# Performance work log

Measured on AMD Instinct MI355X. Metric: run time of the kernel, lower is better.

Reference implementation:

```python
import jax, jax.numpy as jnp
import numpy as np

NEGPOS_RATIO = 3


def setup_inputs() -> dict:
    key = jax.random.key(0)
    k1, k2, k3 = jax.random.split(key, 3)
    B, P, NUM_ATTR, NUM_CLASSES = 64, 32768, 14, 10
    p = jax.random.normal(k1, (B, P, NUM_ATTR), dtype=jnp.float32)
    loc_t = jax.random.normal(k2, (B, P, 4), dtype=jnp.float32)
    conf_t = jax.random.randint(k3, (B, P), 0, NUM_CLASSES, dtype=jnp.int32)
    return {"p": p, "loc_t": loc_t, "conf_t": conf_t}


def reference(p, loc_t, conf_t):
    # p: [B, P, 4 + num_classes] concatenated loc + conf predictions
    loc_p = p[:, :, :4]
    conf_p = p[:, :, 4:]
    B, P = conf_t.shape

    pos = conf_t > 0                       # [B, P] positive anchor mask
    num_pos = jnp.sum(pos)                 # global scalar, as in original

    # Smooth-L1 (beta=1) summed over positive anchors
    diff = loc_p - loc_t
    ad = jnp.abs(diff)
    sl1 = jnp.where(ad < 1.0, 0.5 * diff * diff, ad - 0.5)
    loss_loc = jnp.sum(sl1 * pos[..., None].astype(sl1.dtype))

    # Per-anchor CE-style confidence loss: logsumexp - logit[target]
    lse = jax.nn.logsumexp(conf_p, axis=-1)                      # [B, P]
    tgt_logit = jnp.take_along_axis(conf_p, conf_t[..., None].astype(jnp.int32), axis=-1)[..., 0]
    ce_all = lse - tgt_logit                                     # [B, P]

    # Hard negative mining: zero positives, rank descending per image
    loss_c = jnp.where(pos, 0.0, ce_all)
    order = jnp.argsort(-loss_c, axis=1)   # descending sort indices
    rank = jnp.argsort(order, axis=1)      # rank of each anchor
    num_neg = jnp.clip(NEGPOS_RATIO * num_pos, None, P - num_pos)
    neg = rank < num_neg                   # [B, P]

    sel = pos | neg
    loss_c_sum = jnp.sum(ce_all * sel.astype(ce_all.dtype))

    return (loss_loc + loss_c_sum) / num_pos.astype(p.dtype)
```

## Files before the change

### kernel.cpp

```cpp
#include <hip/hip_runtime.h>

#define NB 64
#define NP 32768
#define NA 14
#define NC 10
#define NANCH (NB * NP)
#define TILE 256
#define TPB 4
#define MAIN_BLOCKS (NANCH / (TILE * TPB))

#define ACC_LOSS  (2 * MAIN_BLOCKS)
#define ACC_NPOS  (2 * MAIN_BLOCKS + 1)
#define DONE_SLOT (2 * MAIN_BLOCKS + 2)

typedef const __attribute__((address_space(1))) void* gptr_t;
typedef __attribute__((address_space(3))) void* lptr_t;

__global__ __launch_bounds__(256) void ssd_main(
    const float* __restrict__ p,
    const float* __restrict__ loc_t,
    const int* __restrict__ conf_t,
    double* __restrict__ ws)
{
    __shared__ float sp[2][TILE * NA];

    const int tid  = threadIdx.x;
    const int lane = tid & 63, wid = tid >> 6;
    const size_t tile0 = (size_t)blockIdx.x * TPB;

    auto stage = [&](int b, size_t tidx) {
        const char* gsrc  = reinterpret_cast<const char*>(p + tidx * (TILE * NA));
        char*       sbase = reinterpret_cast<char*>(sp[b]);
#pragma unroll
        for (int k = 0; k < 3; ++k) {
            const int c0 = k * 256 + wid * 64;
            __builtin_amdgcn_global_load_lds(
                (gptr_t)(gsrc + (size_t)(c0 + lane) * 16),
                (lptr_t)(sbase + (size_t)c0 * 16), 16, 0, 0);
        }
        if (wid < 2) {
            const int c0 = 768 + wid * 64;
            __builtin_amdgcn_global_load_lds(
                (gptr_t)(gsrc + (size_t)(c0 + lane) * 16),
                (lptr_t)(sbase + (size_t)c0 * 16), 16, 0, 0);
        }
    };

    stage(0, tile0);

    float lossAcc = 0.f;
    int   cntAcc  = 0;

#pragma unroll
    for (int it = 0; it < TPB; ++it) {
        const size_t abase = (tile0 + it) * TILE;
        float4 lt = reinterpret_cast<const float4*>(loc_t)[abase + tid];
        int t = conf_t[abase + tid];

        __syncthreads();

        if (it + 1 < TPB) stage((it + 1) & 1, tile0 + it + 1);

        const float2* row =
            reinterpret_cast<const float2*>(&sp[it & 1][tid * NA]);
        float x[14];
#pragma unroll
        for (int j = 0; j < 7; ++j) {
            float2 w = row[j];
            x[2 * j]     = w.x;
            x[2 * j + 1] = w.y;
        }

        float m = x[4];
#pragma unroll
        for (int j = 5; j < 14; ++j) m = fmaxf(m, x[j]);
        float s = 0.f;
#pragma unroll
        for (int j = 4; j < 14; ++j) s += __expf(x[j] - m);
        float lse = m + __logf(s);

        float tgt = x[4];
#pragma unroll
        for (int j = 1; j < 10; ++j) tgt = (t == j) ? x[4 + j] : tgt;
        float ce = lse - tgt;

        if (t > 0) {
            float l = ce;
            const float* ltf = reinterpret_cast<const float*>(&lt);
#pragma unroll
            for (int j = 0; j < 4; ++j) {
                float d  = x[j] - ltf[j];
                float ad = fabsf(d);
                l += (ad < 1.f) ? (0.5f * d * d) : (ad - 0.5f);
            }
            lossAcc += l;
            ++cntAcc;
        }
    }

    double dl = (double)lossAcc;
    int cnt = cntAcc;
#pragma unroll
    for (int off = 32; off > 0; off >>= 1) {
        dl  += __shfl_down(dl, off, 64);
        cnt += __shfl_down(cnt, off, 64);
    }
    __shared__ double sL[4];
    __shared__ int    sC[4];
    if (lane == 0) { sL[wid] = dl; sC[wid] = cnt; }
    __syncthreads();
    if (tid == 0) {
        ws[blockIdx.x] = sL[0] + sL[1] + sL[2] + sL[3];
        ws[MAIN_BLOCKS + blockIdx.x] =
            (double)(sC[0] + sC[1] + sC[2] + sC[3]);
    }
}

__global__ __launch_bounds__(256) void ssd_reduce(double* __restrict__ ws,
                                                  float* __restrict__ out)
{
    const int tid = threadIdx.x;
    double l = 0.0, c = 0.0;
    for (int i = tid; i < MAIN_BLOCKS; i += 256) {
        l += ws[i];
        c += ws[MAIN_BLOCKS + i];
    }
#pragma unroll
    for (int off = 32; off > 0; off >>= 1) {
        l += __shfl_down(l, off, 64);
        c += __shfl_down(c, off, 64);
    }
    __shared__ double sL[4], sC[4];
    int lane = tid & 63, wid = tid >> 6;
    if (lane == 0) { sL[wid] = l; sC[wid] = c; }
    __syncthreads();
    if (tid == 0) {
        double L  = sL[0] + sL[1] + sL[2] + sL[3];
        double np = sC[0] + sC[1] + sC[2] + sC[3];
        ws[ACC_LOSS] = L;
        ws[ACC_NPOS] = np;
        *reinterpret_cast<unsigned long long*>(ws + DONE_SLOT) = 0ull;
        long long npi = (long long)np;
        long long nn = 3 * npi;
        long long ub = (long long)NP - npi;
        if (ub < nn) nn = ub;
        if (nn <= 0) out[0] = (float)(L / np);
    }
}

__device__ __forceinline__ float neg_conf_loss(
    const float* __restrict__ prow, const int* __restrict__ crow, int i)
{
    int t = crow[i];
    if (t > 0) return 0.f;
    const float* v = prow + (size_t)i * NA + 4;
    float m = v[0];
#pragma unroll
    for (int j = 1; j < NC; ++j) m = fmaxf(m, v[j]);
    float s = 0.f;
#pragma unroll
    for (int j = 0; j < NC; ++j) s += __expf(v[j] - m);
    return (m + __logf(s)) - v[0];
}

__global__ __launch_bounds__(256) void ssd_mine(
    const float* __restrict__ p,
    const int* __restrict__ conf_t,
    double* __restrict__ ws,
    float* __restrict__ out)
{
    const double np_d = ws[ACC_NPOS];
    long long np = (long long)np_d;
    long long nn = 3 * np;
    long long ub = (long long)NP - np;
    if (ub < nn) nn = ub;
    if (nn <= 0) return;

    const int tid = threadIdx.x;
    int lane = tid & 63, wid = tid >> 6;
    const float* prow = p + (size_t)blockIdx.x * NP * NA;
    const int*   crow = conf_t + (size_t)blockIdx.x * NP;

    __shared__ unsigned int hist[256];
    __shared__ unsigned int s_prefix;
    __shared__ long long    s_want;

    unsigned int prefix = 0;
    long long want = nn;

    for (int pass = 0; pass < 4; ++pass) {
        int shift = 24 - 8 * pass;
        hist[tid] = 0;
        __syncthreads();
        for (int i = tid; i < NP; i += 256) {
            unsigned int k = __float_as_uint(neg_conf_loss(prow, crow, i));
            bool match = (pass == 0) || ((k >> (shift + 8)) == prefix);
            if (match) atomicAdd(&hist[(k >> shift) & 255u], 1u);
        }
        __syncthreads();
        if (tid == 0) {
            unsigned long long cum = 0;
            int d = 255;
            for (; d > 0; --d) {
                unsigned long long h = hist[d];
                if (cum + h >= (unsigned long long)want) break;
                cum += h;
            }
            s_want   = want - (long long)cum;
            s_prefix = (prefix << 8) | (unsigned int)d;
        }
        __syncthreads();
        prefix = s_prefix;
        want   = s_want;
        __syncthreads();
    }

    float T = __uint_as_float(prefix);
    double sgt = 0.0;
    long long cgt = 0;
    for (int i = tid; i < NP; i += 256) {
        float lc = neg_conf_loss(prow, crow, i);
        if (__float_as_uint(lc) > prefix) { sgt += (double)lc; ++cgt; }
    }
#pragma unroll
    for (int off = 32; off > 0; off >>= 1) {
        sgt += __shfl_down(sgt, off, 64);
        cgt += __shfl_down(cgt, off, 64);
    }
    __shared__ double    rL[4];
    __shared__ long long rC[4];
    if (lane == 0) { rL[wid] = sgt; rC[wid] = cgt; }
    __syncthreads();
    if (tid == 0) {
        double stot = rL[0] + rL[1] + rL[2] + rL[3];
        long long ctot = rC[0] + rC[1] + rC[2] + rC[3];
        double rowsum = stot + (double)(nn - ctot) * (double)T;
        atomicAdd(&ws[ACC_LOSS], rowsum);
    }

    __threadfence();
    __shared__ unsigned int s_ticket;
    if (tid == 0)
        s_ticket = atomicAdd(reinterpret_cast<unsigned int*>(ws + DONE_SLOT), 1u);
    __syncthreads();
    if (s_ticket == NB - 1 && tid == 0) {
        double total = __hip_atomic_load(&ws[ACC_LOSS], __ATOMIC_RELAXED,
                                         __HIP_MEMORY_SCOPE_AGENT);
        out[0] = (float)(total / np_d);
    }
}

extern "C" void kernel_launch(void* const* d_in, const int* in_sizes, int n_in,
                              void* d_out, int out_size, void* d_ws, size_t ws_size,
                              hipStream_t stream)
{
    const float* p      = (const float*)d_in[0];
    const float* loc_t  = (const float*)d_in[1];
    const int*   conf_t = (const int*)d_in[2];
    float*  out = (float*)d_out;
    double* ws  = (double*)d_ws;

    ssd_main<<<MAIN_BLOCKS, 256, 0, stream>>>(p, loc_t, conf_t, ws);
    ssd_reduce<<<1, 256, 0, stream>>>(ws, out);
    ssd_mine<<<NB, 256, 0, stream>>>(p, conf_t, ws, out);
}
```

Measured before the change: 34.65 us.

## Merge reduce kernel into mining kernel, prefetch labels, double tiles per block

Removes the single-block reduce launch by having every mining block re-sum the per-block positive counts itself, with block 0 also summing the base loss and the last-ticket block combining results. Workspace initialization moves into the main kernel. The main kernel now prefetches the next tile's loc_t and conf_t one iteration ahead and processes 8 tiles per block instead of 4. Each of the 64 mining blocks now redundantly reads the per-block count array, and the larger tile count halves the main kernel's block count, which may reduce occupancy.

```diff
diff --git a/kernel.cpp b/kernel.cpp
--- a/kernel.cpp
+++ b/kernel.cpp
@@ -6,11 +6,11 @@
 #define NC 10
 #define NANCH (NB * NP)
 #define TILE 256
-#define TPB 4
+#define TPB 8
 #define MAIN_BLOCKS (NANCH / (TILE * TPB))
 
 #define ACC_LOSS  (2 * MAIN_BLOCKS)
-#define ACC_NPOS  (2 * MAIN_BLOCKS + 1)
+#define ACC_MINE  (2 * MAIN_BLOCKS + 1)
 #define DONE_SLOT (2 * MAIN_BLOCKS + 2)
 
 typedef const __attribute__((address_space(1))) void* gptr_t;
@@ -28,6 +28,11 @@
     const int lane = tid & 63, wid = tid >> 6;
     const size_t tile0 = (size_t)blockIdx.x * TPB;
 
+    if (blockIdx.x == 0 && tid == 0) {
+        ws[ACC_MINE] = 0.0;
+        *reinterpret_cast<unsigned long long*>(ws + DONE_SLOT) = 0ull;
+    }
+
     auto stage = [&](int b, size_t tidx) {
         const char* gsrc  = reinterpret_cast<const char*>(p + tidx * (TILE * NA));
         char*       sbase = reinterpret_cast<char*>(sp[b]);
@@ -47,19 +52,23 @@
     };
 
     stage(0, tile0);
+    float4 ltc = reinterpret_cast<const float4*>(loc_t)[tile0 * TILE + tid];
+    int    tc  = conf_t[tile0 * TILE + tid];
 
     float lossAcc = 0.f;
     int   cntAcc  = 0;
 
 #pragma unroll
     for (int it = 0; it < TPB; ++it) {
-        const size_t abase = (tile0 + it) * TILE;
-        float4 lt = reinterpret_cast<const float4*>(loc_t)[abase + tid];
-        int t = conf_t[abase + tid];
-
-        __syncthreads();
-
-        if (it + 1 < TPB) stage((it + 1) & 1, tile0 + it + 1);
+        __syncthreads();
+
+        float4 ltn = ltc; int tn = tc;
+        if (it + 1 < TPB) {
+            stage((it + 1) & 1, tile0 + it + 1);
+            const size_t nb = (tile0 + it + 1) * TILE;
+            ltn = reinterpret_cast<const float4*>(loc_t)[nb + tid];
+            tn  = conf_t[nb + tid];
+        }
 
         const float2* row =
             reinterpret_cast<const float2*>(&sp[it & 1][tid * NA]);
@@ -81,12 +90,12 @@
 
         float tgt = x[4];
 #pragma unroll
-        for (int j = 1; j < 10; ++j) tgt = (t == j) ? x[4 + j] : tgt;
+        for (int j = 1; j < 10; ++j) tgt = (tc == j) ? x[4 + j] : tgt;
         float ce = lse - tgt;
 
-        if (t > 0) {
+        if (tc > 0) {
             float l = ce;
-            const float* ltf = reinterpret_cast<const float*>(&lt);
+            const float* ltf = reinterpret_cast<const float*>(&ltc);
 #pragma unroll
             for (int j = 0; j < 4; ++j) {
                 float d  = x[j] - ltf[j];
@@ -96,6 +105,7 @@
             lossAcc += l;
             ++cntAcc;
         }
+        ltc = ltn; tc = tn;
     }
 
     double dl = (double)lossAcc;
@@ -116,38 +126,6 @@
     }
 }
 
-__global__ __launch_bounds__(256) void ssd_reduce(double* __restrict__ ws,
-                                                  float* __restrict__ out)
-{
-    const int tid = threadIdx.x;
-    double l = 0.0, c = 0.0;
-    for (int i = tid; i < MAIN_BLOCKS; i += 256) {
-        l += ws[i];
-        c += ws[MAIN_BLOCKS + i];
-    }
-#pragma unroll
-    for (int off = 32; off > 0; off >>= 1) {
-        l += __shfl_down(l, off, 64);
-        c += __shfl_down(c, off, 64);
-    }
-    __shared__ double sL[4], sC[4];
-    int lane = tid & 63, wid = tid >> 6;
-    if (lane == 0) { sL[wid] = l; sC[wid] = c; }
-    __syncthreads();
-    if (tid == 0) {
-        double L  = sL[0] + sL[1] + sL[2] + sL[3];
-        double np = sC[0] + sC[1] + sC[2] + sC[3];
-        ws[ACC_LOSS] = L;
-        ws[ACC_NPOS] = np;
-        *reinterpret_cast<unsigned long long*>(ws + DONE_SLOT) = 0ull;
-        long long npi = (long long)np;
-        long long nn = 3 * npi;
-        long long ub = (long long)NP - npi;
-        if (ub < nn) nn = ub;
-        if (nn <= 0) out[0] = (float)(L / np);
-    }
-}
-
 __device__ __forceinline__ float neg_conf_loss(
     const float* __restrict__ prow, const int* __restrict__ crow, int i)
 {
@@ -163,21 +141,55 @@
     return (m + __logf(s)) - v[0];
 }
 
-__global__ __launch_bounds__(256) void ssd_mine(
+__global__ __launch_bounds__(256) void ssd_finish(
     const float* __restrict__ p,
     const int* __restrict__ conf_t,
     double* __restrict__ ws,
     float* __restrict__ out)
 {
-    const double np_d = ws[ACC_NPOS];
+    const int tid = threadIdx.x;
+    const int lane = tid & 63, wid = tid >> 6;
+    __shared__ double sR[4];
+    __shared__ double s_np;
+
+    double c = 0.0;
+    for (int i = tid; i < MAIN_BLOCKS; i += 256)
+        c += ws[MAIN_BLOCKS + i];
+#pragma unroll
+    for (int off = 32; off > 0; off >>= 1)
+        c += __shfl_down(c, off, 64);
+    if (lane == 0) sR[wid] = c;
+    __syncthreads();
+    if (tid == 0) s_np = sR[0] + sR[1] + sR[2] + sR[3];
+    __syncthreads();
+    const double np_d = s_np;
+
     long long np = (long long)np_d;
     long long nn = 3 * np;
     long long ub = (long long)NP - np;
     if (ub < nn) nn = ub;
-    if (nn <= 0) return;
-
-    const int tid = threadIdx.x;
-    int lane = tid & 63, wid = tid >> 6;
+
+    auto base_loss = [&]() -> double {
+        double l = 0.0;
+        for (int i = tid; i < MAIN_BLOCKS; i += 256)
+            l += ws[i];
+#pragma unroll
+        for (int off = 32; off > 0; off >>= 1)
+            l += __shfl_down(l, off, 64);
+        __shared__ double fL[4];
+        if (lane == 0) fL[wid] = l;
+        __syncthreads();
+        return fL[0] + fL[1] + fL[2] + fL[3];
+    };
+
+    if (nn <= 0) {
+        if (blockIdx.x == 0) {
+            double L = base_loss();
+            if (tid == 0) out[0] = (float)(L / np_d);
+        }
+        return;
+    }
+
     const float* prow = p + (size_t)blockIdx.x * NP * NA;
     const int*   crow = conf_t + (size_t)blockIdx.x * NP;
 
@@ -235,7 +247,12 @@
         double stot = rL[0] + rL[1] + rL[2] + rL[3];
         long long ctot = rC[0] + rC[1] + rC[2] + rC[3];
         double rowsum = stot + (double)(nn - ctot) * (double)T;
-        atomicAdd(&ws[ACC_LOSS], rowsum);
+        atomicAdd(&ws[ACC_MINE], rowsum);
+    }
+
+    if (blockIdx.x == 0) {
+        double L = base_loss();
+        if (tid == 0) ws[ACC_LOSS] = L;
     }
 
     __threadfence();
@@ -244,9 +261,11 @@
         s_ticket = atomicAdd(reinterpret_cast<unsigned int*>(ws + DONE_SLOT), 1u);
     __syncthreads();
     if (s_ticket == NB - 1 && tid == 0) {
-        double total = __hip_atomic_load(&ws[ACC_LOSS], __ATOMIC_RELAXED,
+        double base  = __hip_atomic_load(&ws[ACC_LOSS], __ATOMIC_RELAXED,
                                          __HIP_MEMORY_SCOPE_AGENT);
-        out[0] = (float)(total / np_d);
+        double mined = __hip_atomic_load(&ws[ACC_MINE], __ATOMIC_RELAXED,
+                                         __HIP_MEMORY_SCOPE_AGENT);
+        out[0] = (float)((base + mined) / np_d);
     }
 }
 
@@ -261,6 +280,5 @@
     double* ws  = (double*)d_ws;
 
     ssd_main<<<MAIN_BLOCKS, 256, 0, stream>>>(p, loc_t, conf_t, ws);
-    ssd_reduce<<<1, 256, 0, stream>>>(ws, out);
-    ssd_mine<<<NB, 256, 0, stream>>>(p, conf_t, ws, out);
-}
+    ssd_finish<<<NB, 256, 0, stream>>>(p, conf_t, ws, out);
+}
```

Result: faster. 33.57 us (-3.1%).
